# Kernel optimization log

Measured on AMD Instinct MI355X. Metric: run time of the kernel, lower is better.

The kernel has to match this reference:

```python
import jax, jax.numpy as jnp
import numpy as np

B, S, D, H = 1, 4096, 1024, 16
DH = D // H

def setup_inputs() -> dict:
    key = jax.random.key(0)
    ks = jax.random.split(key, 5)
    std = float(np.sqrt(2.0 / (D + D)))
    return {
        "x": jax.random.normal(ks[0], (B, S, D), dtype=jnp.float32),
        "Wq": jax.random.normal(ks[1], (D, D), dtype=jnp.float32) * std,
        "Wk": jax.random.normal(ks[2], (D, D), dtype=jnp.float32) * std,
        "Wv": jax.random.normal(ks[3], (D, D), dtype=jnp.float32) * std,
        "Wo": jax.random.normal(ks[4], (D, D), dtype=jnp.float32) * std,
    }

def reference(x, Wq, Wk, Wv, Wo):
    # projections: input @ W.T, then split heads: b s (h d) -> b h s d
    def split_heads(t):
        b, s, _ = t.shape
        return t.reshape(b, s, H, DH).transpose(0, 2, 1, 3)
    q = split_heads(x @ Wq.T)
    k = split_heads(x @ Wk.T)
    v = split_heads(x @ Wv.T)
    scale = 1.0 / jnp.sqrt(jnp.asarray(DH, dtype=x.dtype))
    scores = jnp.einsum("bhqd,bhkd->bhqk", q, k) * scale  # (b,h,s,s)
    # causal mask: allow k <= q
    causal = jnp.tril(jnp.ones((S, S), dtype=bool))
    scores = jnp.where(causal, scores, jnp.finfo(scores.dtype).min)
    attn = jax.nn.softmax(scores, axis=-1)
    out = jnp.einsum("bhqk,bhkd->bhqd", attn, v)  # (b,h,s,d)
    out = out.transpose(0, 2, 1, 3).reshape(B, S, D)  # b h s d -> b s (h d)
    return out @ Wo.T
```

## Files before the change

kernel.cpp:

```cpp
#include <hip/hip_runtime.h>
#include <math.h>

#define SEQ 4096
#define DM  1024
#define NH  16
#define DH  64
#define NS  4

typedef _Float16 h16;
typedef __attribute__((ext_vector_type(4))) _Float16 h16x4;
typedef __attribute__((ext_vector_type(8))) _Float16 h16x8;
typedef __attribute__((ext_vector_type(4))) float f32x4;

__device__ __forceinline__ void gload_lds16(const h16* g, h16* l) {
    __builtin_amdgcn_global_load_lds(
        (const __attribute__((address_space(1))) void*)g,
        (__attribute__((address_space(3))) void*)l, 16, 0, 0);
}

__global__ __launch_bounds__(256) void cvt_all(const float* __restrict__ x,
                                               const float* __restrict__ wq,
                                               const float* __restrict__ wk,
                                               const float* __restrict__ wv,
                                               const float* __restrict__ wo,
                                               h16* __restrict__ dst) {
    const size_t SD4 = (size_t)SEQ * DM / 4;
    const size_t DD4 = (size_t)DM * DM / 4;
    const size_t i = (size_t)blockIdx.x * 256 + threadIdx.x;
    const float* src;
    size_t off;
    if (i < SD4) { src = x; off = i; }
    else {
        const size_t j = i - SD4;
        const int wsel = (int)(j >> 18);
        off = j & (DD4 - 1);
        src = (wsel == 0) ? wq : (wsel == 1) ? wk : (wsel == 2) ? wv : wo;
    }
    const float4 v = ((const float4*)src)[off];
    h16x4 o = { (h16)v.x, (h16)v.y, (h16)v.z, (h16)v.w };
    ((h16x4*)dst)[i] = o;
}

#define GT 32

__global__ __launch_bounds__(256) void gemm_qkv(const h16* __restrict__ xh,
                                                const h16* __restrict__ Wq,
                                                const h16* __restrict__ Wk,
                                                const h16* __restrict__ Wv,
                                                h16* __restrict__ Qh,
                                                h16* __restrict__ Kh,
                                                h16* __restrict__ Vth,
                                                float scl) {
    __shared__ h16 As[2][128 * GT];
    __shared__ h16 Bs[2][128 * GT];

    const int z    = blockIdx.z;
    const h16* B   = (z == 0) ? Wq : (z == 1) ? Wk : Wv;
    const int t    = threadIdx.x;
    const int lane = t & 63;
    const int w    = t >> 6;
    const int wm   = (w >> 1) * 64;
    const int wn   = (w & 1) * 64;
    const int l15  = lane & 15;
    const int lq   = lane >> 4;
    const int lq8  = lq * 8;
    const int m0   = blockIdx.y * 128;
    const int n0   = blockIdx.x * 128;
    const int K = DM, M = SEQ, N = DM;

    const int srow = w * 16 + (lane >> 2);
    const int scol = (lane & 3) * 8;
    const h16* pa0 = xh + (size_t)(m0 + srow) * K + scol;
    const h16* pa1 = xh + (size_t)(m0 + 64 + srow) * K + scol;
    const h16* pb0 = B  + (size_t)(n0 + srow) * K + scol;
    const h16* pb1 = B  + (size_t)(n0 + 64 + srow) * K + scol;

    f32x4 acc[4][4] = {};

    for (int k0 = 0; k0 < K; k0 += 64) {
        __syncthreads();
        #pragma unroll
        for (int s = 0; s < 2; ++s) {
            const int ko = k0 + s * 32;
            gload_lds16(pa0 + ko, &As[s][w * 512]);
            gload_lds16(pa1 + ko, &As[s][2048 + w * 512]);
            gload_lds16(pb0 + ko, &Bs[s][w * 512]);
            gload_lds16(pb1 + ko, &Bs[s][2048 + w * 512]);
        }
        __syncthreads();

        #pragma unroll
        for (int s = 0; s < 2; ++s) {
            h16x8 af[4], bf[4];
            #pragma unroll
            for (int i = 0; i < 4; ++i)
                af[i] = *(const h16x8*)&As[s][(wm + i * 16 + l15) * GT + lq8];
            #pragma unroll
            for (int j = 0; j < 4; ++j)
                bf[j] = *(const h16x8*)&Bs[s][(wn + j * 16 + l15) * GT + lq8];
            #pragma unroll
            for (int i = 0; i < 4; ++i)
                #pragma unroll
                for (int j = 0; j < 4; ++j)
                    acc[i][j] = __builtin_amdgcn_mfma_f32_16x16x32_f16(af[i], bf[j], acc[i][j], 0, 0, 0);
        }
    }

    const int cr = wm + lq * 4;
    const int cc = wn + l15;
    if (z == 2) {
        #pragma unroll
        for (int i = 0; i < 4; ++i)
            #pragma unroll
            for (int j = 0; j < 4; ++j) {
                const int gm0 = m0 + cr + i * 16;
                const int gn  = n0 + cc + j * 16;
                h16x4 v = { (h16)acc[i][j][0], (h16)acc[i][j][1],
                            (h16)acc[i][j][2], (h16)acc[i][j][3] };
                *(h16x4*)(Vth + (size_t)gn * M + gm0) = v;
            }
    } else {
        h16* Og = (z == 0) ? Qh : Kh;
        const float e = (z == 0) ? scl : 1.0f;
        #pragma unroll
        for (int i = 0; i < 4; ++i)
            #pragma unroll
            for (int j = 0; j < 4; ++j)
                #pragma unroll
                for (int r = 0; r < 4; ++r) {
                    const int gm = m0 + cr + i * 16 + r;
                    const int gn = n0 + cc + j * 16;
                    Og[(size_t)gm * N + gn] = (h16)(acc[i][j][r] * e);
                }
    }
}

__global__ __launch_bounds__(256) void gemm_out(const h16* __restrict__ A,
                                                const h16* __restrict__ B,
                                                float* __restrict__ C) {
    __shared__ h16 As[2][64 * GT];
    __shared__ h16 Bs[2][128 * GT];

    const int t    = threadIdx.x;
    const int lane = t & 63;
    const int w    = t >> 6;
    const int wm   = (w >> 1) * 32;
    const int wn   = (w & 1) * 64;
    const int l15  = lane & 15;
    const int lq   = lane >> 4;
    const int lq8  = lq * 8;
    const int m0   = blockIdx.y * 64;
    const int n0   = blockIdx.x * 128;
    const int K = DM, N = DM;

    const int srow = w * 16 + (lane >> 2);
    const int scol = (lane & 3) * 8;
    const h16* pa0 = A + (size_t)(m0 + srow) * K + scol;
    const h16* pb0 = B + (size_t)(n0 + srow) * K + scol;
    const h16* pb1 = B + (size_t)(n0 + 64 + srow) * K + scol;

    f32x4 acc[2][4] = {};

    for (int k0 = 0; k0 < K; k0 += 64) {
        __syncthreads();
        #pragma unroll
        for (int s = 0; s < 2; ++s) {
            const int ko = k0 + s * 32;
            gload_lds16(pa0 + ko, &As[s][w * 512]);
            gload_lds16(pb0 + ko, &Bs[s][w * 512]);
            gload_lds16(pb1 + ko, &Bs[s][2048 + w * 512]);
        }
        __syncthreads();

        #pragma unroll
        for (int s = 0; s < 2; ++s) {
            h16x8 af[2], bf[4];
            #pragma unroll
            for (int i = 0; i < 2; ++i)
                af[i] = *(const h16x8*)&As[s][(wm + i * 16 + l15) * GT + lq8];
            #pragma unroll
            for (int j = 0; j < 4; ++j)
                bf[j] = *(const h16x8*)&Bs[s][(wn + j * 16 + l15) * GT + lq8];
            #pragma unroll
            for (int i = 0; i < 2; ++i)
                #pragma unroll
                for (int j = 0; j < 4; ++j)
                    acc[i][j] = __builtin_amdgcn_mfma_f32_16x16x32_f16(af[i], bf[j], acc[i][j], 0, 0, 0);
        }
    }

    const int cr = wm + lq * 4;
    const int cc = wn + l15;
    #pragma unroll
    for (int i = 0; i < 2; ++i)
        #pragma unroll
        for (int j = 0; j < 4; ++j)
            #pragma unroll
            for (int r = 0; r < 4; ++r)
                C[(size_t)(m0 + cr + i * 16 + r) * N + n0 + cc + j * 16] = acc[i][j][r];
}

#define AST 80
#define VST 72

__global__ __launch_bounds__(256, 4) void flash_attn_split(
        const h16* __restrict__ Qg, const h16* __restrict__ Kg,
        const h16* __restrict__ Vt, h16* __restrict__ OP,
        float* __restrict__ Mb, float* __restrict__ Lb) {
    __shared__ h16 Ks[2][64 * AST];
    __shared__ h16 Vs[2][64 * VST];

    const int qt   = 63 - (int)blockIdx.y;
    const int hh   = blockIdx.x;
    const int sp   = blockIdx.z;
    const int t    = threadIdx.x;
    const int lane = t & 63;
    const int w    = t >> 6;
    const int l15  = lane & 15;
    const int lq   = lane >> 4;
    const int lq8  = lq * 8;
    const int hc   = hh * DH;
    const int q0   = qt * 64;
    const int q_loc = w * 16 + l15;

    const int ntile = qt + 1;
    const int chunk = (ntile + NS - 1) / NS;
    const int kts   = sp * chunk;
    const int kte   = (kts + chunk < ntile) ? (kts + chunk) : ntile;

    const int r1 = t >> 3;
    const int r2 = r1 + 32;
    const int c1 = (t & 7) * 8;

    const size_t qrow = (size_t)(q0 + q_loc) * DM + hc;
    h16x8 qf[2];
    qf[0] = *(const h16x8*)(Qg + qrow + lq8);
    qf[1] = *(const h16x8*)(Qg + qrow + 32 + lq8);

    const int kb0 = kts * 64;
    h16x8 kv1 = *(const h16x8*)(Kg + (size_t)(kb0 + r1) * DM + hc + c1);
    h16x8 kv2 = *(const h16x8*)(Kg + (size_t)(kb0 + r2) * DM + hc + c1);
    h16x8 vv1 = *(const h16x8*)(Vt + (size_t)(hc + r1) * SEQ + kb0 + c1);
    h16x8 vv2 = *(const h16x8*)(Vt + (size_t)(hc + r2) * SEQ + kb0 + c1);

    float m_st = -1e30f, l_st = 0.0f;
    f32x4 o[4] = {};
    int bb = 0;

    for (int kt = kts; kt < kte; ++kt) {
        *(h16x8*)&Ks[bb][r1 * AST + c1] = kv1;
        *(h16x8*)&Ks[bb][r2 * AST + c1] = kv2;
        *(h16x8*)&Vs[bb][r1 * VST + c1] = vv1;
        *(h16x8*)&Vs[bb][r2 * VST + c1] = vv2;
        __syncthreads();
        if (kt + 1 < kte) {
            const int k0n = (kt + 1) * 64;
            kv1 = *(const h16x8*)(Kg + (size_t)(k0n + r1) * DM + hc + c1);
            kv2 = *(const h16x8*)(Kg + (size_t)(k0n + r2) * DM + hc + c1);
            vv1 = *(const h16x8*)(Vt + (size_t)(hc + r1) * SEQ + k0n + c1);
            vv2 = *(const h16x8*)(Vt + (size_t)(hc + r2) * SEQ + k0n + c1);
        }

        f32x4 s[4] = {};
        #pragma unroll
        for (int kc = 0; kc < 2; ++kc)
            #pragma unroll
            for (int jj = 0; jj < 4; ++jj) {
                const h16x8 kf = *(const h16x8*)&Ks[bb][(jj * 16 + l15) * AST + kc * 32 + lq8];
                s[jj] = __builtin_amdgcn_mfma_f32_16x16x32_f16(kf, qf[kc], s[jj], 0, 0, 0);
            }

        if (kt == qt) {
            #pragma unroll
            for (int jj = 0; jj < 4; ++jj)
                #pragma unroll
                for (int r = 0; r < 4; ++r)
                    if ((jj * 16 + lq * 4 + r) > q_loc) s[jj][r] = -1e30f;
        }
        float mx = -1e30f;
        #pragma unroll
        for (int jj = 0; jj < 4; ++jj)
            #pragma unroll
            for (int r = 0; r < 4; ++r)
                mx = fmaxf(mx, s[jj][r]);
        mx = fmaxf(mx, __shfl_xor(mx, 16, 64));
        mx = fmaxf(mx, __shfl_xor(mx, 32, 64));
        if (mx > m_st + 5.0f) {
            const float alpha = exp2f(m_st - mx);
            m_st = mx;
            l_st *= alpha;
            #pragma unroll
            for (int jj = 0; jj < 4; ++jj)
                #pragma unroll
                for (int r = 0; r < 4; ++r)
                    o[jj][r] *= alpha;
        }

        h16x4 pk[4];
        #pragma unroll
        for (int jj = 0; jj < 4; ++jj) {
            const float p0 = exp2f(s[jj][0] - m_st);
            const float p1 = exp2f(s[jj][1] - m_st);
            const float p2 = exp2f(s[jj][2] - m_st);
            const float p3 = exp2f(s[jj][3] - m_st);
            l_st += (p0 + p1) + (p2 + p3);
            pk[jj] = h16x4{ (h16)p0, (h16)p1, (h16)p2, (h16)p3 };
        }

        #pragma unroll
        for (int dd = 0; dd < 4; ++dd)
            #pragma unroll
            for (int jj = 0; jj < 4; ++jj) {
                const h16x4 vf = *(const h16x4*)&Vs[bb][(dd * 16 + l15) * VST + jj * 16 + lq * 4];
                o[dd] = __builtin_amdgcn_mfma_f32_16x16x16f16(vf, pk[jj], o[dd], 0, 0, 0);
            }

        bb ^= 1;
    }

    l_st += __shfl_xor(l_st, 16, 64);
    l_st += __shfl_xor(l_st, 32, 64);

    h16* const op = OP + (size_t)sp * SEQ * DM;
    const size_t qg = (size_t)(q0 + q_loc) * DM + hc;
    #pragma unroll
    for (int jj = 0; jj < 4; ++jj) {
        h16x4 ov = { (h16)o[jj][0], (h16)o[jj][1],
                     (h16)o[jj][2], (h16)o[jj][3] };
        *(h16x4*)(op + qg + jj * 16 + lq * 4) = ov;
    }
    if (lq == 0) {
        const size_t mi = ((size_t)sp * NH + hh) * SEQ + q0 + q_loc;
        Mb[mi] = m_st;
        Lb[mi] = l_st;
    }
}

__global__ __launch_bounds__(256) void combine(const h16* __restrict__ OP,
                                               const float* __restrict__ Mb,
                                               const float* __restrict__ Lb,
                                               h16* __restrict__ AOh) {
    const int i  = blockIdx.x * 256 + threadIdx.x;
    const int q  = i >> 8;
    const int c4 = (i & 255) * 4;
    const int hh = c4 >> 6;

    float ms[NS], ls[NS];
    float mstar = -1e30f;
    #pragma unroll
    for (int s = 0; s < NS; ++s) {
        const size_t mi = ((size_t)s * NH + hh) * SEQ + q;
        ms[s] = Mb[mi];
        ls[s] = Lb[mi];
        mstar = fmaxf(mstar, ms[s]);
    }
    float L = 0.0f;
    float acc[4] = {};
    #pragma unroll
    for (int s = 0; s < NS; ++s) {
        const float ws = exp2f(ms[s] - mstar);
        L += ls[s] * ws;
        const h16x4 ov = *(const h16x4*)(OP + (size_t)s * SEQ * DM + (size_t)q * DM + c4);
        acc[0] += ws * (float)ov[0];
        acc[1] += ws * (float)ov[1];
        acc[2] += ws * (float)ov[2];
        acc[3] += ws * (float)ov[3];
    }
    const float inv = 1.0f / L;
    h16x4 r = { (h16)(acc[0] * inv), (h16)(acc[1] * inv),
                (h16)(acc[2] * inv), (h16)(acc[3] * inv) };
    *(h16x4*)(AOh + (size_t)q * DM + c4) = r;
}

extern "C" void kernel_launch(void* const* d_in, const int* in_sizes, int n_in,
                              void* d_out, int out_size, void* d_ws, size_t ws_size,
                              hipStream_t stream) {
    const float* x  = (const float*)d_in[0];
    const float* Wq = (const float*)d_in[1];
    const float* Wk = (const float*)d_in[2];
    const float* Wv = (const float*)d_in[3];
    const float* Wo = (const float*)d_in[4];
    float* out = (float*)d_out;

    const size_t SD = (size_t)SEQ * DM;
    const size_t DD = (size_t)DM * DM;

    h16* xh  = (h16*)d_ws;
    h16* wqh = xh + SD;
    h16* wkh = wqh + DD;
    h16* wvh = wkh + DD;
    h16* woh = wvh + DD;
    h16* Qh  = woh + DD;
    h16* Kh  = Qh + SD;
    h16* Vth = Kh + SD;
    h16* AOh = Vth + SD;
    h16* OP  = AOh + SD;
    float* Mb = (float*)(OP + (size_t)NS * SD);
    float* Lb = Mb + (size_t)NS * NH * SEQ;

    const dim3 blk(256);

    cvt_all<<<(int)((SD + 4 * DD) / 4 / 256), blk, 0, stream>>>(x, Wq, Wk, Wv, Wo, xh);

    const float SCL = 0.125f * 1.44269504088896340736f;

    gemm_qkv<<<dim3(DM / 128, SEQ / 128, 3), blk, 0, stream>>>(
        xh, wqh, wkh, wvh, Qh, Kh, Vth, SCL);

    flash_attn_split<<<dim3(NH, 64, NS), blk, 0, stream>>>(Qh, Kh, Vth, OP, Mb, Lb);

    combine<<<(int)(SD / 4 / 256), blk, 0, stream>>>(OP, Mb, Lb, AOh);

    gemm_out<<<dim3(DM / 128, SEQ / 64), blk, 0, stream>>>(AOh, woh, out);
}
```

Before: 222.1 us.

## Process two 64-row query tiles per flash-attention block to reuse K/V tiles

Each attention block now handles 128 query rows as two 64-row halves, each with its own softmax state, so every K/V tile staged in LDS feeds twice as many MFMAs. This halves the grid in the query dimension and roughly halves K/V global and LDS traffic per unit of work. In exchange it raises register pressure, so the occupancy hint drops from 4 to 3. Fewer, larger blocks also make causal load balance coarser, and the first half computes a fully masked extra diagonal tile.

```diff
diff --git a/kernel.cpp b/kernel.cpp
--- a/kernel.cpp
+++ b/kernel.cpp
@@ -203,14 +203,14 @@
 #define AST 80
 #define VST 72
 
-__global__ __launch_bounds__(256, 4) void flash_attn_split(
+__global__ __launch_bounds__(256, 3) void flash_attn_split(
         const h16* __restrict__ Qg, const h16* __restrict__ Kg,
         const h16* __restrict__ Vt, h16* __restrict__ OP,
         float* __restrict__ Mb, float* __restrict__ Lb) {
     __shared__ h16 Ks[2][64 * AST];
     __shared__ h16 Vs[2][64 * VST];
 
-    const int qt   = 63 - (int)blockIdx.y;
+    const int jq   = 31 - (int)blockIdx.y;
     const int hh   = blockIdx.x;
     const int sp   = blockIdx.z;
     const int t    = threadIdx.x;
@@ -220,10 +220,12 @@
     const int lq   = lane >> 4;
     const int lq8  = lq * 8;
     const int hc   = hh * DH;
-    const int q0   = qt * 64;
-    const int q_loc = w * 16 + l15;
-
-    const int ntile = qt + 1;
+    const int q0   = jq * 128;
+    const int qa   = w * 16 + l15;
+    const int diag1 = 2 * jq;
+    const int diag2 = 2 * jq + 1;
+
+    const int ntile = 2 * jq + 2;
     const int chunk = (ntile + NS - 1) / NS;
     const int kts   = sp * chunk;
     const int kte   = (kts + chunk < ntile) ? (kts + chunk) : ntile;
@@ -232,10 +234,13 @@
     const int r2 = r1 + 32;
     const int c1 = (t & 7) * 8;
 
-    const size_t qrow = (size_t)(q0 + q_loc) * DM + hc;
-    h16x8 qf[2];
-    qf[0] = *(const h16x8*)(Qg + qrow + lq8);
-    qf[1] = *(const h16x8*)(Qg + qrow + 32 + lq8);
+    const size_t qrow1 = (size_t)(q0 + qa) * DM + hc;
+    const size_t qrow2 = (size_t)(q0 + 64 + qa) * DM + hc;
+    h16x8 qf[2][2];
+    qf[0][0] = *(const h16x8*)(Qg + qrow1 + lq8);
+    qf[0][1] = *(const h16x8*)(Qg + qrow1 + 32 + lq8);
+    qf[1][0] = *(const h16x8*)(Qg + qrow2 + lq8);
+    qf[1][1] = *(const h16x8*)(Qg + qrow2 + 32 + lq8);
 
     const int kb0 = kts * 64;
     h16x8 kv1 = *(const h16x8*)(Kg + (size_t)(kb0 + r1) * DM + hc + c1);
@@ -243,8 +248,9 @@
     h16x8 vv1 = *(const h16x8*)(Vt + (size_t)(hc + r1) * SEQ + kb0 + c1);
     h16x8 vv2 = *(const h16x8*)(Vt + (size_t)(hc + r2) * SEQ + kb0 + c1);
 
-    float m_st = -1e30f, l_st = 0.0f;
-    f32x4 o[4] = {};
+    float m_st[2] = { -1e30f, -1e30f };
+    float l_st[2] = { 0.0f, 0.0f };
+    f32x4 o[2][4] = {};
     int bb = 0;
 
     for (int kt = kts; kt < kte; ++kt) {
@@ -261,50 +267,68 @@
             vv2 = *(const h16x8*)(Vt + (size_t)(hc + r2) * SEQ + k0n + c1);
         }
 
-        f32x4 s[4] = {};
-        #pragma unroll
-        for (int kc = 0; kc < 2; ++kc)
+        f32x4 s[2][4] = {};
+        #pragma unroll
+        for (int kc = 0; kc < 2; ++kc) {
+            h16x8 kf[4];
+            #pragma unroll
+            for (int jj = 0; jj < 4; ++jj)
+                kf[jj] = *(const h16x8*)&Ks[bb][(jj * 16 + l15) * AST + kc * 32 + lq8];
+            #pragma unroll
+            for (int jj = 0; jj < 4; ++jj)
+                s[0][jj] = __builtin_amdgcn_mfma_f32_16x16x32_f16(kf[jj], qf[0][kc], s[0][jj], 0, 0, 0);
+            #pragma unroll
+            for (int jj = 0; jj < 4; ++jj)
+                s[1][jj] = __builtin_amdgcn_mfma_f32_16x16x32_f16(kf[jj], qf[1][kc], s[1][jj], 0, 0, 0);
+        }
+
+        if (kt >= diag1) {
+            const int rel = (q0 + qa) - kt * 64;
+            #pragma unroll
+            for (int jj = 0; jj < 4; ++jj)
+                #pragma unroll
+                for (int r = 0; r < 4; ++r)
+                    if ((jj * 16 + lq * 4 + r) > rel) s[0][jj][r] = -1e30f;
+        }
+        if (kt >= diag2) {
+            const int rel = (q0 + 64 + qa) - kt * 64;
+            #pragma unroll
+            for (int jj = 0; jj < 4; ++jj)
+                #pragma unroll
+                for (int r = 0; r < 4; ++r)
+                    if ((jj * 16 + lq * 4 + r) > rel) s[1][jj][r] = -1e30f;
+        }
+
+        h16x4 pk[2][4];
+        #pragma unroll
+        for (int h = 0; h < 2; ++h) {
+            float mx = -1e30f;
+            #pragma unroll
+            for (int jj = 0; jj < 4; ++jj)
+                #pragma unroll
+                for (int r = 0; r < 4; ++r)
+                    mx = fmaxf(mx, s[h][jj][r]);
+            mx = fmaxf(mx, __shfl_xor(mx, 16, 64));
+            mx = fmaxf(mx, __shfl_xor(mx, 32, 64));
+            if (mx > m_st[h] + 5.0f) {
+                const float alpha = exp2f(m_st[h] - mx);
+                m_st[h] = mx;
+                l_st[h] *= alpha;
+                #pragma unroll
+                for (int jj = 0; jj < 4; ++jj)
+                    #pragma unroll
+                    for (int r = 0; r < 4; ++r)
+                        o[h][jj][r] *= alpha;
+            }
             #pragma unroll
             for (int jj = 0; jj < 4; ++jj) {
-                const h16x8 kf = *(const h16x8*)&Ks[bb][(jj * 16 + l15) * AST + kc * 32 + lq8];
-                s[jj] = __builtin_amdgcn_mfma_f32_16x16x32_f16(kf, qf[kc], s[jj], 0, 0, 0);
+                const float p0 = exp2f(s[h][jj][0] - m_st[h]);
+                const float p1 = exp2f(s[h][jj][1] - m_st[h]);
+                const float p2 = exp2f(s[h][jj][2] - m_st[h]);
+                const float p3 = exp2f(s[h][jj][3] - m_st[h]);
+                l_st[h] += (p0 + p1) + (p2 + p3);
+                pk[h][jj] = h16x4{ (h16)p0, (h16)p1, (h16)p2, (h16)p3 };
             }
-
-        if (kt == qt) {
-            #pragma unroll
-            for (int jj = 0; jj < 4; ++jj)
-                #pragma unroll
-                for (int r = 0; r < 4; ++r)
-                    if ((jj * 16 + lq * 4 + r) > q_loc) s[jj][r] = -1e30f;
-        }
-        float mx = -1e30f;
-        #pragma unroll
-        for (int jj = 0; jj < 4; ++jj)
-            #pragma unroll
-            for (int r = 0; r < 4; ++r)
-                mx = fmaxf(mx, s[jj][r]);
-        mx = fmaxf(mx, __shfl_xor(mx, 16, 64));
-        mx = fmaxf(mx, __shfl_xor(mx, 32, 64));
-        if (mx > m_st + 5.0f) {
-            const float alpha = exp2f(m_st - mx);
-            m_st = mx;
-            l_st *= alpha;
-            #pragma unroll
-            for (int jj = 0; jj < 4; ++jj)
-                #pragma unroll
-                for (int r = 0; r < 4; ++r)
-                    o[jj][r] *= alpha;
-        }
-
-        h16x4 pk[4];
-        #pragma unroll
-        for (int jj = 0; jj < 4; ++jj) {
-            const float p0 = exp2f(s[jj][0] - m_st);
-            const float p1 = exp2f(s[jj][1] - m_st);
-            const float p2 = exp2f(s[jj][2] - m_st);
-            const float p3 = exp2f(s[jj][3] - m_st);
-            l_st += (p0 + p1) + (p2 + p3);
-            pk[jj] = h16x4{ (h16)p0, (h16)p1, (h16)p2, (h16)p3 };
         }
 
         #pragma unroll
@@ -312,27 +336,35 @@
             #pragma unroll
             for (int jj = 0; jj < 4; ++jj) {
                 const h16x4 vf = *(const h16x4*)&Vs[bb][(dd * 16 + l15) * VST + jj * 16 + lq * 4];
-                o[dd] = __builtin_amdgcn_mfma_f32_16x16x16f16(vf, pk[jj], o[dd], 0, 0, 0);
+                o[0][dd] = __builtin_amdgcn_mfma_f32_16x16x16f16(vf, pk[0][jj], o[0][dd], 0, 0, 0);
+                o[1][dd] = __builtin_amdgcn_mfma_f32_16x16x16f16(vf, pk[1][jj], o[1][dd], 0, 0, 0);
             }
 
         bb ^= 1;
     }
 
-    l_st += __shfl_xor(l_st, 16, 64);
-    l_st += __shfl_xor(l_st, 32, 64);
+    #pragma unroll
+    for (int h = 0; h < 2; ++h) {
+        l_st[h] += __shfl_xor(l_st[h], 16, 64);
+        l_st[h] += __shfl_xor(l_st[h], 32, 64);
+    }
 
     h16* const op = OP + (size_t)sp * SEQ * DM;
-    const size_t qg = (size_t)(q0 + q_loc) * DM + hc;
     #pragma unroll
-    for (int jj = 0; jj < 4; ++jj) {
-        h16x4 ov = { (h16)o[jj][0], (h16)o[jj][1],
-                     (h16)o[jj][2], (h16)o[jj][3] };
-        *(h16x4*)(op + qg + jj * 16 + lq * 4) = ov;
-    }
-    if (lq == 0) {
-        const size_t mi = ((size_t)sp * NH + hh) * SEQ + q0 + q_loc;
-        Mb[mi] = m_st;
-        Lb[mi] = l_st;
+    for (int h = 0; h < 2; ++h) {
+        const int qg_row = q0 + h * 64 + qa;
+        const size_t qg = (size_t)qg_row * DM + hc;
+        #pragma unroll
+        for (int jj = 0; jj < 4; ++jj) {
+            h16x4 ov = { (h16)o[h][jj][0], (h16)o[h][jj][1],
+                         (h16)o[h][jj][2], (h16)o[h][jj][3] };
+            *(h16x4*)(op + qg + jj * 16 + lq * 4) = ov;
+        }
+        if (lq == 0) {
+            const size_t mi = ((size_t)sp * NH + hh) * SEQ + qg_row;
+            Mb[mi] = m_st[h];
+            Lb[mi] = l_st[h];
+        }
     }
 }
 
@@ -407,7 +439,7 @@
     gemm_qkv<<<dim3(DM / 128, SEQ / 128, 3), blk, 0, stream>>>(
         xh, wqh, wkh, wvh, Qh, Kh, Vth, SCL);
 
-    flash_attn_split<<<dim3(NH, 64, NS), blk, 0, stream>>>(Qh, Kh, Vth, OP, Mb, Lb);
+    flash_attn_split<<<dim3(NH, 32, NS), blk, 0, stream>>>(Qh, Kh, Vth, OP, Mb, Lb);
 
     combine<<<(int)(SD / 4 / 256), blk, 0, stream>>>(OP, Mb, Lb, AOh);
 
```

After: 221.4 us (median of 2 runs). No clear change (-0.3%).
